# Optimization experiments

Hardware: AMD Instinct MI355X
Metric: run time of the kernel (lower is better)

Reference implementation:

```python
import jax, jax.numpy as jnp
import numpy as np
import math

N_EMBD = 1024
N_HEAD = 16
BLOCK_SIZE = 2048
B, T = 4, 2048

def setup_inputs() -> dict:
    key = jax.random.key(0)
    ks = jax.random.split(key, 5)
    s = 0.02
    x = jax.random.normal(ks[0], (B, T, N_EMBD), dtype=jnp.float32)
    W_attn = jax.random.normal(ks[1], (N_EMBD, 3 * N_EMBD), dtype=jnp.float32) * s
    b_attn = jnp.zeros((3 * N_EMBD,), dtype=jnp.float32)
    W_proj = jax.random.normal(ks[2], (N_EMBD, N_EMBD), dtype=jnp.float32) * s
    b_proj = jnp.zeros((N_EMBD,), dtype=jnp.float32)
    return {"x": x, "W_attn": W_attn, "b_attn": b_attn, "W_proj": W_proj, "b_proj": b_proj}

def reference(x, W_attn, b_attn, W_proj, b_proj):
    b, t, c = x.shape
    hd = c // N_HEAD  # head dim
    qkv = x @ W_attn + b_attn                      # [B,T,3C]
    q, k, v = jnp.split(qkv, 3, axis=-1)
    # [B,T,C] -> [B,H,T,hd]
    q = q.reshape(b, t, N_HEAD, hd).transpose(0, 2, 1, 3)
    k = k.reshape(b, t, N_HEAD, hd).transpose(0, 2, 1, 3)
    v = v.reshape(b, t, N_HEAD, hd).transpose(0, 2, 1, 3)
    att = jnp.einsum('bhqd,bhkd->bhqk', q, k) * (1.0 / math.sqrt(hd))
    causal = jnp.tril(jnp.ones((t, t), dtype=bool))
    att = jnp.where(causal[None, None], att, -jnp.inf)
    att = jax.nn.softmax(att, axis=-1)
    y = jnp.einsum('bhqk,bhkd->bhqd', att, v)      # [B,H,T,hd]
    y = y.transpose(0, 2, 1, 3).reshape(b, t, c)
    return y @ W_proj + b_proj
```

## Files before the change

kernel.cpp:

```cpp
#include <hip/hip_runtime.h>

typedef unsigned short u16;
typedef __bf16 bf16x8 __attribute__((ext_vector_type(8)));
typedef float    f32x4 __attribute__((ext_vector_type(4)));
typedef unsigned short u16x8 __attribute__((ext_vector_type(8)));

__device__ __forceinline__ float bf2f(u16 v){ return __uint_as_float(((unsigned int)v) << 16); }
__device__ __forceinline__ u16 f2bf(float f){
    unsigned int u = __float_as_uint(f);
    u += 0x7fffu + ((u >> 16) & 1u);
    return (u16)(u >> 16);
}

__device__ __forceinline__ void glds16(const u16* gp, u16* lp){
    __builtin_amdgcn_global_load_lds((unsigned int __attribute__((address_space(1)))*)gp,
                                     (unsigned int __attribute__((address_space(3)))*)lp,
                                     16, 0, 0);
}

__device__ __forceinline__ int probe_f32(const u16* __restrict__ xp){
    u16 lo = xp[2 * (threadIdx.x & 63)];
    int e = (lo >> 7) & 0xff;
    bool bad = !(e == 0 || (e > 96 && e < 160));
    return __popcll(__ballot(bad)) > 16;
}

__global__ __launch_bounds__(256) void conv_x(const void* __restrict__ src, u16* __restrict__ dst,
                                              const u16* __restrict__ xprobe){
    const int isf32 = probe_f32(xprobe);
    size_t i = ((size_t)blockIdx.x * 256 + threadIdx.x) * 8;
    if (isf32){
        const float* p = (const float*)src + i;
        float4 a = *(const float4*)p, b = *(const float4*)(p + 4);
        u16x8 o = { f2bf(a.x), f2bf(a.y), f2bf(a.z), f2bf(a.w),
                    f2bf(b.x), f2bf(b.y), f2bf(b.z), f2bf(b.w) };
        *(u16x8*)(dst + i) = o;
    } else {
        *(u16x8*)(dst + i) = *(const u16x8*)((const u16*)src + i);
    }
}

__global__ __launch_bounds__(256) void transposeW(const void* __restrict__ in, u16* __restrict__ out,
                                                  int R, int C, const u16* __restrict__ xprobe){
    __shared__ u16 t[64][65];
    const int isf32 = probe_f32(xprobe);
    const int c0 = blockIdx.x * 64, r0 = blockIdx.y * 64;
    const int tx = threadIdx.x & 15, ty = threadIdx.x >> 4;
#pragma unroll
    for (int i = 0; i < 4; i++){
        int r = ty + i * 16;
        u16 a, b, c, d;
        if (isf32){
            float4 v = *(const float4*)((const float*)in + (size_t)(r0 + r) * C + c0 + tx * 4);
            a = f2bf(v.x); b = f2bf(v.y); c = f2bf(v.z); d = f2bf(v.w);
        } else {
            ushort4 v = *(const ushort4*)((const u16*)in + (size_t)(r0 + r) * C + c0 + tx * 4);
            a = v.x; b = v.y; c = v.z; d = v.w;
        }
        t[r][tx*4+0] = a; t[r][tx*4+1] = b; t[r][tx*4+2] = c; t[r][tx*4+3] = d;
    }
    __syncthreads();
#pragma unroll
    for (int i = 0; i < 4; i++){
        int oc = ty + i * 16;
        ushort4 v;
        v.x = t[tx*4+0][oc]; v.y = t[tx*4+1][oc]; v.z = t[tx*4+2][oc]; v.w = t[tx*4+3][oc];
        *(ushort4*)(out + (size_t)(c0 + oc) * R + r0 + tx * 4) = v;
    }
}

template<int MODE>
__global__ __launch_bounds__(256) void gemm128(
    const u16* __restrict__ A, const u16* __restrict__ Bt, const void* __restrict__ bias,
    void* __restrict__ C, u16* __restrict__ Cq, u16* __restrict__ Ck, u16* __restrict__ Cv,
    const u16* __restrict__ xprobe, int M, int N, int K)
{
    __shared__ u16 Asm[128 * 32];
    __shared__ u16 Bsm[128 * 32];
    const int isf32 = probe_f32(xprobe);
    const int tid = threadIdx.x;
    const int wave = tid >> 6, lane = tid & 63;
    const int quad = lane >> 4, ml = lane & 15;
    const int m_blk = blockIdx.y * 128;
    const int n_blk = blockIdx.x * 128;
    const int wm = (wave >> 1) * 64, wn = (wave & 1) * 64;
    const int rsub = lane >> 2;
    const int kc   = lane & 3;

    f32x4 acc[4][4];
#pragma unroll
    for (int a = 0; a < 4; a++)
#pragma unroll
        for (int b = 0; b < 4; b++)
            acc[a][b] = (f32x4){0.f, 0.f, 0.f, 0.f};

    for (int k0 = 0; k0 < K; k0 += 32){
        __syncthreads();
#pragma unroll
        for (int i = 0; i < 2; i++){
            int row = (wave * 2 + i) * 16 + rsub;
            glds16(A  + (size_t)(m_blk + row) * K + k0 + kc * 8, Asm + (wave * 2 + i) * 512);
            glds16(Bt + (size_t)(n_blk + row) * K + k0 + kc * 8, Bsm + (wave * 2 + i) * 512);
        }
        __syncthreads();
        bf16x8 af[4], bfr[4];
#pragma unroll
        for (int mt = 0; mt < 4; mt++) af[mt]  = *(const bf16x8*)&Asm[(wm + mt * 16 + ml) * 32 + quad * 8];
#pragma unroll
        for (int nt = 0; nt < 4; nt++) bfr[nt] = *(const bf16x8*)&Bsm[(wn + nt * 16 + ml) * 32 + quad * 8];
#pragma unroll
        for (int mt = 0; mt < 4; mt++)
#pragma unroll
            for (int nt = 0; nt < 4; nt++)
                acc[mt][nt] = __builtin_amdgcn_mfma_f32_16x16x32_bf16(af[mt], bfr[nt], acc[mt][nt], 0, 0, 0);
    }

    const float QSC = 0.18033688f;
#pragma unroll
    for (int nt = 0; nt < 4; nt++){
        int col = n_blk + wn + nt * 16 + ml;
        float bv = isf32 ? ((const float*)bias)[col] : bf2f(((const u16*)bias)[col]);
#pragma unroll
        for (int mt = 0; mt < 4; mt++){
            float o0 = acc[mt][nt][0] + bv, o1 = acc[mt][nt][1] + bv;
            float o2 = acc[mt][nt][2] + bv, o3 = acc[mt][nt][3] + bv;
            int row0 = m_blk + wm + mt * 16 + quad * 4;
            if (MODE == 0){
                int which = col >> 10;
                int h = (col >> 6) & 15;
                int d = col & 63;
                int b = row0 >> 11, tt = row0 & 2047;
                size_t bh = (size_t)((b << 4) + h);
                if (which == 2){
                    ushort4 o4 = { f2bf(o0), f2bf(o1), f2bf(o2), f2bf(o3) };
                    *(ushort4*)&Cv[(bh * 64 + d) * 2048 + tt] = o4;
                } else if (which == 0){
                    u16* p = Cq + (bh * 2048 + tt) * 64 + d;
                    p[0] = f2bf(o0 * QSC); p[64] = f2bf(o1 * QSC);
                    p[128] = f2bf(o2 * QSC); p[192] = f2bf(o3 * QSC);
                } else {
                    u16* p = Ck + (bh * 2048 + tt) * 64 + d;
                    p[0] = f2bf(o0); p[64] = f2bf(o1); p[128] = f2bf(o2); p[192] = f2bf(o3);
                }
            } else {
                if (isf32){
                    float* p = (float*)C + (size_t)row0 * N + col;
                    p[0] = o0; p[N] = o1; p[2*N] = o2; p[3*N] = o3;
                } else {
                    u16* p = (u16*)C + (size_t)row0 * N + col;
                    p[0] = f2bf(o0); p[N] = f2bf(o1); p[2*N] = f2bf(o2); p[3*N] = f2bf(o3);
                }
            }
        }
    }
}

#define PS 136
__global__ __launch_bounds__(256) void attn_kernel(
    const u16* __restrict__ Q, const u16* __restrict__ K, const u16* __restrict__ Vt,
    u16* __restrict__ Y)
{
    __shared__ u16 Ksm[128 * 64];
    __shared__ u16 Vsm[64 * 128];
    __shared__ u16 Psm[4][32 * PS];

    const int tid = threadIdx.x, wave = tid >> 6, lane = tid & 63;
    const int quad = lane >> 4, ml = lane & 15;
    const int flat = blockIdx.x;
    const int qb = 15 - (flat >> 6);
    const int rest = flat & 63;
    const int bh = ((rest & 7) << 3) | (rest >> 3);
    const int q0 = qb * 128;
    const size_t base = (size_t)bh * (2048 * 64);
    const float NEG = -1.0e30f;

    bf16x8 qf[2][2];
#pragma unroll
    for (int mt = 0; mt < 2; mt++)
#pragma unroll
        for (int ks = 0; ks < 2; ks++)
            qf[mt][ks] = *(const bf16x8*)(Q + base + (size_t)(q0 + mt * 64 + wave * 16 + ml) * 64 + ks * 32 + quad * 8);

    f32x4 acc[2][4];
#pragma unroll
    for (int mt = 0; mt < 2; mt++)
#pragma unroll
        for (int nt = 0; nt < 4; nt++) acc[mt][nt] = (f32x4){0.f, 0.f, 0.f, 0.f};
    float l[2][4];
#pragma unroll
    for (int mt = 0; mt < 2; mt++)
#pragma unroll
        for (int r = 0; r < 4; r++) l[mt][r] = 0.f;

    const int ntj = qb + 1;
    for (int j = 0; j < ntj; j++){
        const int j0 = j * 128;
        __syncthreads();
#pragma unroll
        for (int i = 0; i < 4; i++){
            int ub = i * 256 + wave * 64;
            int u = ub + lane;
            int row = u >> 3, cg = (lane & 7) ^ (row & 7);
            glds16(K + base + (size_t)(j0 + row) * 64 + cg * 8, Ksm + ub * 8);
            int d = u >> 4, vg = (lane & 15) ^ (d & 15);
            glds16(Vt + base + (size_t)d * 2048 + j0 + vg * 8, Vsm + ub * 8);
        }
        __syncthreads();
        const bool lastj = (j == ntj - 1);

#pragma unroll
        for (int nt = 0; nt < 8; nt++){
            bf16x8 bk0 = *(const bf16x8*)&Ksm[(nt * 16 + ml) * 64 + ((quad)     ^ (ml & 7)) * 8];
            bf16x8 bk1 = *(const bf16x8*)&Ksm[(nt * 16 + ml) * 64 + ((4 + quad) ^ (ml & 7)) * 8];
            f32x4 z = {0.f, 0.f, 0.f, 0.f};
            f32x4 s0 = __builtin_amdgcn_mfma_f32_16x16x32_bf16(qf[0][0], bk0, z, 0, 0, 0);
            s0 = __builtin_amdgcn_mfma_f32_16x16x32_bf16(qf[0][1], bk1, s0, 0, 0, 0);
            f32x4 s1 = __builtin_amdgcn_mfma_f32_16x16x32_bf16(qf[1][0], bk0, z, 0, 0, 0);
            s1 = __builtin_amdgcn_mfma_f32_16x16x32_bf16(qf[1][1], bk1, s1, 0, 0, 0);
            if (lastj){
                int cl = nt * 16 + ml;
                int r0 = wave * 16 + quad * 4;
#pragma unroll
                for (int r = 0; r < 4; r++){
                    if (cl > r0 + r)      s0[r] = NEG;
                    if (cl > 64 + r0 + r) s1[r] = NEG;
                }
            }
#pragma unroll
            for (int r = 0; r < 4; r++){
                float p0 = exp2f(s0[r]); l[0][r] += p0;
                Psm[wave][(quad * 4 + r) * PS + nt * 16 + ml] = f2bf(p0);
                float p1 = exp2f(s1[r]); l[1][r] += p1;
                Psm[wave][(16 + quad * 4 + r) * PS + nt * 16 + ml] = f2bf(p1);
            }
        }
#pragma unroll
        for (int ks = 0; ks < 4; ks++){
            bf16x8 pf0 = *(const bf16x8*)&Psm[wave][ml * PS + ks * 32 + quad * 8];
            bf16x8 pf1 = *(const bf16x8*)&Psm[wave][(16 + ml) * PS + ks * 32 + quad * 8];
#pragma unroll
            for (int nt = 0; nt < 4; nt++){
                bf16x8 vf = *(const bf16x8*)&Vsm[(nt * 16 + ml) * 128 + (((ks * 4 + quad) ^ ml) & 15) * 8];
                acc[0][nt] = __builtin_amdgcn_mfma_f32_16x16x32_bf16(pf0, vf, acc[0][nt], 0, 0, 0);
                acc[1][nt] = __builtin_amdgcn_mfma_f32_16x16x32_bf16(pf1, vf, acc[1][nt], 0, 0, 0);
            }
        }
    }
    const int b = bh >> 4, h = bh & 15;
#pragma unroll
    for (int mt = 0; mt < 2; mt++){
        f32x4 inv;
#pragma unroll
        for (int r = 0; r < 4; r++){
            float t = l[mt][r];
            t += __shfl_xor(t, 1, 64);
            t += __shfl_xor(t, 2, 64);
            t += __shfl_xor(t, 4, 64);
            t += __shfl_xor(t, 8, 64);
            inv[r] = 1.0f / t;
        }
#pragma unroll
        for (int nt = 0; nt < 4; nt++)
#pragma unroll
            for (int r = 0; r < 4; r++){
                size_t row = (size_t)b * 2048 + q0 + mt * 64 + wave * 16 + quad * 4 + r;
                Y[row * 1024 + h * 64 + nt * 16 + ml] = f2bf(acc[mt][nt][r] * inv[r]);
            }
    }
}

extern "C" void kernel_launch(void* const* d_in, const int* in_sizes, int n_in,
                              void* d_out, int out_size, void* d_ws, size_t ws_size,
                              hipStream_t stream) {
    const void* x      = d_in[0];
    const void* W_attn = d_in[1];
    const void* b_attn = d_in[2];
    const void* W_proj = d_in[3];
    const void* b_proj = d_in[4];
    const u16* xprobe = (const u16*)x;

    u16* ws = (u16*)d_ws;
    u16* Qw = ws;
    u16* Kw = ws + 8u * 1024 * 1024;
    u16* Vw = ws + 16u * 1024 * 1024;
    u16* R  = ws + 24u * 1024 * 1024;
    u16* Wt_attn = R;
    u16* Yw      = R;
    u16* Wt_proj = Qw;
    u16* xb = (u16*)d_out;

    conv_x<<<4096, 256, 0, stream>>>(x, xb, xprobe);
    transposeW<<<dim3(48, 16), 256, 0, stream>>>(W_attn, Wt_attn, 1024, 3072, xprobe);
    gemm128<0><<<dim3(24, 64), 256, 0, stream>>>(
        xb, Wt_attn, b_attn, nullptr, Qw, Kw, Vw, xprobe, 8192, 3072, 1024);
    attn_kernel<<<1024, 256, 0, stream>>>(Qw, Kw, Vw, Yw);
    transposeW<<<dim3(16, 16), 256, 0, stream>>>(W_proj, Wt_proj, 1024, 1024, xprobe);
    gemm128<1><<<dim3(8, 64), 256, 0, stream>>>(
        Yw, Wt_proj, b_proj, d_out, nullptr, nullptr, nullptr, xprobe, 8192, 1024, 1024);
}
```

Measured before the change: 290.8 us.

## Stage QKV GEMM epilogue through LDS and interleave attention P chunks

The QKV GEMM epilogue now writes each tile into an LDS transpose buffer and then stores it to Q/K/V with 16-byte coalesced writes, replacing scattered 2-byte stores. In attention, the probability tile is built and consumed in 32-column chunks, so the per-wave P buffer shrinks and PV MFMAs interleave with QK work. exp2f becomes raw v_exp_f32 and bf16 rounding becomes truncation, which cuts ALU work but slightly changes numerics. The extra 34KB of LDS in the GEMM may reduce occupancy.

```diff
diff --git a/kernel.cpp b/kernel.cpp
--- a/kernel.cpp
+++ b/kernel.cpp
@@ -10,6 +10,13 @@
     unsigned int u = __float_as_uint(f);
     u += 0x7fffu + ((u >> 16) & 1u);
     return (u16)(u >> 16);
+}
+__device__ __forceinline__ u16 f2bf_t(float f){ return (u16)(__float_as_uint(f) >> 16); }
+__device__ __forceinline__ unsigned pack_trunc(float hi, float lo){
+    return __builtin_amdgcn_perm(__float_as_uint(hi), __float_as_uint(lo), 0x07060302);
+}
+__device__ __forceinline__ float exp2_fast(float x){
+    float r; asm("v_exp_f32 %0, %1" : "=v"(r) : "v"(x)); return r;
 }
 
 __device__ __forceinline__ void glds16(const u16* gp, u16* lp){
@@ -69,6 +76,7 @@
     }
 }
 
+#define CTS 136
 template<int MODE>
 __global__ __launch_bounds__(256) void gemm128(
     const u16* __restrict__ A, const u16* __restrict__ Bt, const void* __restrict__ bias,
@@ -77,6 +85,7 @@
 {
     __shared__ u16 Asm[128 * 32];
     __shared__ u16 Bsm[128 * 32];
+    __shared__ u16 Ct[128 * CTS];
     const int isf32 = probe_f32(xprobe);
     const int tid = threadIdx.x;
     const int wave = tid >> 6, lane = tid & 63;
@@ -116,33 +125,69 @@
     }
 
     const float QSC = 0.18033688f;
-#pragma unroll
-    for (int nt = 0; nt < 4; nt++){
-        int col = n_blk + wn + nt * 16 + ml;
-        float bv = isf32 ? ((const float*)bias)[col] : bf2f(((const u16*)bias)[col]);
-#pragma unroll
-        for (int mt = 0; mt < 4; mt++){
-            float o0 = acc[mt][nt][0] + bv, o1 = acc[mt][nt][1] + bv;
-            float o2 = acc[mt][nt][2] + bv, o3 = acc[mt][nt][3] + bv;
-            int row0 = m_blk + wm + mt * 16 + quad * 4;
-            if (MODE == 0){
-                int which = col >> 10;
-                int h = (col >> 6) & 15;
-                int d = col & 63;
-                int b = row0 >> 11, tt = row0 & 2047;
-                size_t bh = (size_t)((b << 4) + h);
-                if (which == 2){
-                    ushort4 o4 = { f2bf(o0), f2bf(o1), f2bf(o2), f2bf(o3) };
-                    *(ushort4*)&Cv[(bh * 64 + d) * 2048 + tt] = o4;
-                } else if (which == 0){
-                    u16* p = Cq + (bh * 2048 + tt) * 64 + d;
-                    p[0] = f2bf(o0 * QSC); p[64] = f2bf(o1 * QSC);
-                    p[128] = f2bf(o2 * QSC); p[192] = f2bf(o3 * QSC);
-                } else {
-                    u16* p = Ck + (bh * 2048 + tt) * 64 + d;
-                    p[0] = f2bf(o0); p[64] = f2bf(o1); p[128] = f2bf(o2); p[192] = f2bf(o3);
-                }
-            } else {
+    if (MODE == 0){
+        const int which = n_blk >> 10;
+        const int hbase = (n_blk >> 6) & 15;
+        if (which < 2){
+            const float sc = (which == 0) ? QSC : 1.0f;
+#pragma unroll
+            for (int nt = 0; nt < 4; nt++){
+                int col = wn + nt * 16 + ml;
+                float bv = isf32 ? ((const float*)bias)[n_blk + col] : bf2f(((const u16*)bias)[n_blk + col]);
+#pragma unroll
+                for (int mt = 0; mt < 4; mt++){
+                    int row0 = wm + mt * 16 + quad * 4;
+#pragma unroll
+                    for (int r = 0; r < 4; r++)
+                        Ct[(row0 + r) * CTS + col] = f2bf_t((acc[mt][nt][r] + bv) * sc);
+                }
+            }
+            __syncthreads();
+            u16* dst0 = (which == 0) ? Cq : Ck;
+            const int b = m_blk >> 11, t0 = m_blk & 2047;
+#pragma unroll
+            for (int i = 0; i < 8; i++){
+                int u = i * 256 + tid;
+                int row = u >> 4, c8 = u & 15;
+                int h = hbase + (c8 >> 3), d8 = (c8 & 7) * 8;
+                u16x8 v = *(const u16x8*)&Ct[row * CTS + c8 * 8];
+                *(u16x8*)&dst0[(((size_t)(b * 16 + h)) * 2048 + (t0 + row)) * 64 + d8] = v;
+            }
+        } else {
+#pragma unroll
+            for (int nt = 0; nt < 4; nt++){
+                int col = wn + nt * 16 + ml;
+                float bv = isf32 ? ((const float*)bias)[n_blk + col] : bf2f(((const u16*)bias)[n_blk + col]);
+#pragma unroll
+                for (int mt = 0; mt < 4; mt++){
+                    int row0 = wm + mt * 16 + quad * 4;
+                    uint2 pk;
+                    pk.x = pack_trunc(acc[mt][nt][1] + bv, acc[mt][nt][0] + bv);
+                    pk.y = pack_trunc(acc[mt][nt][3] + bv, acc[mt][nt][2] + bv);
+                    *(uint2*)&Ct[col * CTS + row0] = pk;
+                }
+            }
+            __syncthreads();
+            const int b = m_blk >> 11, t0 = m_blk & 2047;
+#pragma unroll
+            for (int i = 0; i < 8; i++){
+                int u = i * 256 + tid;
+                int col = u >> 4, c8 = u & 15;
+                int h = hbase + (col >> 6), d = col & 63;
+                u16x8 v = *(const u16x8*)&Ct[col * CTS + c8 * 8];
+                *(u16x8*)&Cv[(((size_t)(b * 16 + h)) * 64 + d) * 2048 + t0 + c8 * 8] = v;
+            }
+        }
+    } else {
+#pragma unroll
+        for (int nt = 0; nt < 4; nt++){
+            int col = n_blk + wn + nt * 16 + ml;
+            float bv = isf32 ? ((const float*)bias)[col] : bf2f(((const u16*)bias)[col]);
+#pragma unroll
+            for (int mt = 0; mt < 4; mt++){
+                float o0 = acc[mt][nt][0] + bv, o1 = acc[mt][nt][1] + bv;
+                float o2 = acc[mt][nt][2] + bv, o3 = acc[mt][nt][3] + bv;
+                int row0 = m_blk + wm + mt * 16 + quad * 4;
                 if (isf32){
                     float* p = (float*)C + (size_t)row0 * N + col;
                     p[0] = o0; p[N] = o1; p[2*N] = o2; p[3*N] = o3;
@@ -155,14 +200,14 @@
     }
 }
 
-#define PS 136
+#define PSc 40
 __global__ __launch_bounds__(256) void attn_kernel(
     const u16* __restrict__ Q, const u16* __restrict__ K, const u16* __restrict__ Vt,
     u16* __restrict__ Y)
 {
     __shared__ u16 Ksm[128 * 64];
     __shared__ u16 Vsm[64 * 128];
-    __shared__ u16 Psm[4][32 * PS];
+    __shared__ u16 Psm[4][32 * PSc];
 
     const int tid = threadIdx.x, wave = tid >> 6, lane = tid & 63;
     const int quad = lane >> 4, ml = lane & 15;
@@ -209,38 +254,39 @@
         const bool lastj = (j == ntj - 1);
 
 #pragma unroll
-        for (int nt = 0; nt < 8; nt++){
-            bf16x8 bk0 = *(const bf16x8*)&Ksm[(nt * 16 + ml) * 64 + ((quad)     ^ (ml & 7)) * 8];
-            bf16x8 bk1 = *(const bf16x8*)&Ksm[(nt * 16 + ml) * 64 + ((4 + quad) ^ (ml & 7)) * 8];
-            f32x4 z = {0.f, 0.f, 0.f, 0.f};
-            f32x4 s0 = __builtin_amdgcn_mfma_f32_16x16x32_bf16(qf[0][0], bk0, z, 0, 0, 0);
-            s0 = __builtin_amdgcn_mfma_f32_16x16x32_bf16(qf[0][1], bk1, s0, 0, 0, 0);
-            f32x4 s1 = __builtin_amdgcn_mfma_f32_16x16x32_bf16(qf[1][0], bk0, z, 0, 0, 0);
-            s1 = __builtin_amdgcn_mfma_f32_16x16x32_bf16(qf[1][1], bk1, s1, 0, 0, 0);
-            if (lastj){
-                int cl = nt * 16 + ml;
-                int r0 = wave * 16 + quad * 4;
+        for (int ntp = 0; ntp < 4; ntp++){
+#pragma unroll
+            for (int h = 0; h < 2; h++){
+                const int nt = ntp * 2 + h;
+                bf16x8 bk0 = *(const bf16x8*)&Ksm[(nt * 16 + ml) * 64 + ((quad)     ^ (ml & 7)) * 8];
+                bf16x8 bk1 = *(const bf16x8*)&Ksm[(nt * 16 + ml) * 64 + ((4 + quad) ^ (ml & 7)) * 8];
+                f32x4 z = {0.f, 0.f, 0.f, 0.f};
+                f32x4 s0 = __builtin_amdgcn_mfma_f32_16x16x32_bf16(qf[0][0], bk0, z, 0, 0, 0);
+                s0 = __builtin_amdgcn_mfma_f32_16x16x32_bf16(qf[0][1], bk1, s0, 0, 0, 0);
+                f32x4 s1 = __builtin_amdgcn_mfma_f32_16x16x32_bf16(qf[1][0], bk0, z, 0, 0, 0);
+                s1 = __builtin_amdgcn_mfma_f32_16x16x32_bf16(qf[1][1], bk1, s1, 0, 0, 0);
+                if (lastj){
+                    int cl = nt * 16 + ml;
+                    int r0 = wave * 16 + quad * 4;
+#pragma unroll
+                    for (int r = 0; r < 4; r++){
+                        if (cl > r0 + r)      s0[r] = NEG;
+                        if (cl > 64 + r0 + r) s1[r] = NEG;
+                    }
+                }
 #pragma unroll
                 for (int r = 0; r < 4; r++){
-                    if (cl > r0 + r)      s0[r] = NEG;
-                    if (cl > 64 + r0 + r) s1[r] = NEG;
-                }
-            }
-#pragma unroll
-            for (int r = 0; r < 4; r++){
-                float p0 = exp2f(s0[r]); l[0][r] += p0;
-                Psm[wave][(quad * 4 + r) * PS + nt * 16 + ml] = f2bf(p0);
-                float p1 = exp2f(s1[r]); l[1][r] += p1;
-                Psm[wave][(16 + quad * 4 + r) * PS + nt * 16 + ml] = f2bf(p1);
-            }
-        }
-#pragma unroll
-        for (int ks = 0; ks < 4; ks++){
-            bf16x8 pf0 = *(const bf16x8*)&Psm[wave][ml * PS + ks * 32 + quad * 8];
-            bf16x8 pf1 = *(const bf16x8*)&Psm[wave][(16 + ml) * PS + ks * 32 + quad * 8];
+                    float p0 = exp2_fast(s0[r]); l[0][r] += p0;
+                    Psm[wave][(quad * 4 + r) * PSc + h * 16 + ml] = f2bf_t(p0);
+                    float p1 = exp2_fast(s1[r]); l[1][r] += p1;
+                    Psm[wave][(16 + quad * 4 + r) * PSc + h * 16 + ml] = f2bf_t(p1);
+                }
+            }
+            bf16x8 pf0 = *(const bf16x8*)&Psm[wave][ml * PSc + quad * 8];
+            bf16x8 pf1 = *(const bf16x8*)&Psm[wave][(16 + ml) * PSc + quad * 8];
 #pragma unroll
             for (int nt = 0; nt < 4; nt++){
-                bf16x8 vf = *(const bf16x8*)&Vsm[(nt * 16 + ml) * 128 + (((ks * 4 + quad) ^ ml) & 15) * 8];
+                bf16x8 vf = *(const bf16x8*)&Vsm[(nt * 16 + ml) * 128 + (((ntp * 4 + quad) ^ ml) & 15) * 8];
                 acc[0][nt] = __builtin_amdgcn_mfma_f32_16x16x32_bf16(pf0, vf, acc[0][nt], 0, 0, 0);
                 acc[1][nt] = __builtin_amdgcn_mfma_f32_16x16x32_bf16(pf1, vf, acc[1][nt], 0, 0, 0);
             }
```

Measured after the change: 290.2 us. About the same (-0.2%).
